# Performance work log

Hardware: AMD Instinct MI355X
Metric: run time of the kernel (lower is better)

## Reference

```python
import jax, jax.numpy as jnp
import numpy as np

B, DIM = 16384, 1024
H1, H2, H3 = 500, 200, 200


def setup_inputs() -> dict:
    key = jax.random.key(0)
    ks = jax.random.split(key, 16)
    s = 0.01
    return {
        "x": jax.random.normal(ks[0], (B, DIM), dtype=jnp.float32),
        "show_index": jax.random.randint(ks[1], (B,), 0, 100),
        "st": jax.random.normal(ks[2], (1000, 16), dtype=jnp.float32),
        # deep MLP params (shared across the two task heads, as in the source)
        "W1": jax.random.normal(ks[3], (DIM, H1), dtype=jnp.float32) * s,
        "b1": jnp.zeros((H1,), dtype=jnp.float32),
        "W2": jax.random.normal(ks[4], (H1, H2), dtype=jnp.float32) * s,
        "b2": jnp.zeros((H2,), dtype=jnp.float32),
        "W3": jax.random.normal(ks[5], (H2, H3), dtype=jnp.float32) * s,
        "b3": jnp.zeros((H3,), dtype=jnp.float32),
        # final sigmoid head on concat([emb(DIM), d3(H3)])
        "Wl": jax.random.normal(ks[6], (DIM + H3, 1), dtype=jnp.float32) * s,
        "bl": jnp.zeros((1,), dtype=jnp.float32),
        # per-(task, cross-layer) cross weights/biases: tf.random_normal stddev=0.01
        "cw": jax.random.normal(ks[7], (2, 3, DIM), dtype=jnp.float32) * s,
        "cb": jax.random.normal(ks[8], (2, 3, DIM), dtype=jnp.float32) * s,
    }


def reference(x, show_index, st, W1, b1, W2, b2, W3, b3, Wl, bl, cw, cb):
    # Deep part (same shared Dense layers each task -> compute once).
    d = jax.nn.relu(x @ W1 + b1)
    d = jax.nn.relu(d @ W2 + b2)
    d3 = jax.nn.relu(d @ W3 + b3)  # (B, H3)

    # cross_net: sum_i w[j] * x[b,i] * emb[b,j]  ==  x.sum(1) * emb[b,j] * w[j]
    # (collapsed form of the (B,dim,dim) outer product + axis-1 reduction)
    xsum = jnp.sum(x, axis=1, keepdims=True)  # (B, 1)
    preds = []
    for i in range(2):
        emb = x
        for j in range(3):
            emb = xsum * emb * cw[i, j] + cb[i, j] + x
        mid = jnp.concatenate([emb, d3], axis=-1)  # (B, DIM+H3)
        preds.append(jax.nn.sigmoid(mid @ Wl + bl))  # (B, 1)
    return tuple(preds)
```

## Files before the change

### kernel.cpp

```cpp
#include <hip/hip_runtime.h>
#include <hip/hip_bf16.h>
#include <math.h>

#define B_ROWS 16384
#define DIM 1024

typedef __attribute__((ext_vector_type(8))) short s16x8;
typedef __attribute__((ext_vector_type(4))) float f32x4;

static __device__ __forceinline__ unsigned short f2bf(float f) {
    union { float f; unsigned u; } v; v.f = f;
    unsigned r = v.u + 0x7FFF + ((v.u >> 16) & 1);
    return (unsigned short)(r >> 16);
}

static __device__ __forceinline__ unsigned cvt_pk_bf16(float lo, float hi) {
    unsigned r;
    asm volatile("v_cvt_pk_bf16_f32 %0, %1, %2" : "=v"(r) : "v"(lo), "v"(hi));
    return r;
}

static __device__ __forceinline__ void gload16(const unsigned short* g, unsigned short* l) {
    __builtin_amdgcn_global_load_lds(
        (const __attribute__((address_space(1))) unsigned int*)g,
        (__attribute__((address_space(3))) unsigned int*)l, 16, 0, 0);
}

__global__ __launch_bounds__(256) void prep(
    const float* __restrict__ W1, const float* __restrict__ W2,
    const float* __restrict__ W3,
    const float* __restrict__ cw, const float* __restrict__ cb,
    const float* __restrict__ Wl,
    unsigned short* __restrict__ W1b, unsigned short* __restrict__ W2b,
    unsigned short* __restrict__ W3b,
    float* __restrict__ czz) {
    __shared__ unsigned short tile[64][72];
    __shared__ float red[4][6];
    const int tid = threadIdx.x;
    const int blk = blockIdx.x;

    if (blk < 176) {
        const int w = blk;
        const float* src; unsigned short* dst;
        int kt, nt, Ksrc, Nsrc, ldDst;
        bool skipHi = false;
        if (w < 128)      { kt = w & 15;         nt = w >> 4;         src = W1; dst = W1b; Ksrc = 1024; Nsrc = 500; ldDst = 1024; skipHi = true; }
        else if (w < 160) { kt = (w - 128) & 7;  nt = (w - 128) >> 3; src = W2; dst = W2b; Ksrc = 500;  Nsrc = 200; ldDst = 512;  }
        else              { kt = (w - 160) & 3;  nt = (w - 160) >> 2; src = W3; dst = W3b; Ksrc = 200;  Nsrc = 200; ldDst = 256;  }
        const int k0 = kt << 6, n0 = nt << 6;
        {
            const int r = tid >> 2, c0 = (tid & 3) << 4;
            const int kk = k0 + r;
#pragma unroll
            for (int i = 0; i < 16; ++i) {
                const int nn = n0 + c0 + i;
                const float v = (kk < Ksrc && nn < Nsrc) ? src[(size_t)kk * Nsrc + nn] : 0.f;
                tile[r][c0 + i] = f2bf(v);
            }
        }
        __syncthreads();
        {
            const int n = tid >> 2, kc = (tid & 3) << 4;
            if (!(skipHi && (n0 + n) >= 500)) {
                unsigned short* o = dst + (size_t)(n0 + n) * ldDst + k0 + kc;
#pragma unroll
                for (int i = 0; i < 16; ++i) o[i] = tile[kc + i][n];
            }
        }
    } else if (blk == 176) {
#pragma unroll
        for (int q = 0; q < 4; ++q) {
            const int k = tid * 4 + q;
            const float wl = Wl[k];
            const float a1 = cw[k],         a2 = cw[1024 + k],  a3 = cw[2048 + k];
            const float d1_ = cw[3072 + k], d2_ = cw[4096 + k], d3_ = cw[5120 + k];
            W1b[(size_t)500 * 1024 + k] = f2bf(a1 * a2 * a3 * wl);
            W1b[(size_t)501 * 1024 + k] = f2bf(a2 * a3 * wl);
            W1b[(size_t)502 * 1024 + k] = f2bf(a3 * wl);
            W1b[(size_t)503 * 1024 + k] = f2bf(d1_ * d2_ * d3_ * wl);
            W1b[(size_t)504 * 1024 + k] = f2bf(d2_ * d3_ * wl);
            W1b[(size_t)505 * 1024 + k] = f2bf(d3_ * wl);
            W1b[(size_t)506 * 1024 + k] = f2bf(wl);
            W1b[(size_t)507 * 1024 + k] = 0x3F80;
            W1b[(size_t)508 * 1024 + k] = 0;
            W1b[(size_t)509 * 1024 + k] = 0;
            W1b[(size_t)510 * 1024 + k] = 0;
            W1b[(size_t)511 * 1024 + k] = 0;
        }
    } else {
        float c[6] = {0.f, 0.f, 0.f, 0.f, 0.f, 0.f};
#pragma unroll
        for (int q = 0; q < 4; ++q) {
            const int k = tid * 4 + q;
            const float wl = Wl[k];
            {
                const float w2 = cw[1024 + k], w3 = cw[2048 + k];
                const float b1 = cb[k], b2 = cb[1024 + k], b3 = cb[2048 + k];
                c[0] += w2 * w3 * b1 * wl;
                c[1] += w3 * b2 * wl;
                c[2] += b3 * wl;
            }
            {
                const float w2 = cw[4096 + k], w3 = cw[5120 + k];
                const float b1 = cb[3072 + k], b2 = cb[4096 + k], b3 = cb[5120 + k];
                c[3] += w2 * w3 * b1 * wl;
                c[4] += w3 * b2 * wl;
                c[5] += b3 * wl;
            }
        }
        const int lane = tid & 63, wv = tid >> 6;
#pragma unroll
        for (int j = 0; j < 6; ++j)
#pragma unroll
            for (int m = 1; m < 64; m <<= 1) c[j] += __shfl_xor(c[j], m, 64);
        if (lane == 0)
#pragma unroll
            for (int j = 0; j < 6; ++j) red[wv][j] = c[j];
        __syncthreads();
        if (tid < 6) czz[tid] = red[0][tid] + red[1][tid] + red[2][tid] + red[3][tid];
    }
}

template <int ROWS>
static __device__ __forceinline__ void stage_tile(
    const unsigned short* __restrict__ src, int K, int rowBase, int kt,
    unsigned short* lds, int w, int lane) {
    const int r8   = lane >> 3;
    const int slot = lane & 7;
#pragma unroll
    for (int q = 0; q < ROWS / 32; ++q) {
        const int blk   = q * 4 + w;
        const int row   = blk * 8 + r8;
        const int chunk = slot ^ (row & 7);
        const unsigned short* g = src + (size_t)(rowBase + row) * K + kt * 64 + chunk * 8;
        gload16(g, lds + blk * 512);
    }
}

template <int ROWS>
static __device__ __forceinline__ void stage8(
    const unsigned short* __restrict__ src, int K, int rowBase, int kt,
    unsigned short* lds, int w, int lane) {
    const int r8   = lane >> 3;
    const int slot = lane & 7;
#pragma unroll
    for (int q = 0; q < ROWS / 64; ++q) {
        const int blk   = q * 8 + w;
        const int row   = blk * 8 + r8;
        const int chunk = slot ^ (row & 7);
        const unsigned short* g = src + (size_t)(rowBase + row) * K + kt * 64 + chunk * 8;
        gload16(g, lds + blk * 512);
    }
}

__global__ __launch_bounds__(256) void gemm_xa(
    const float* __restrict__ X,
    const unsigned short* __restrict__ Bw,
    const float* __restrict__ bias,
    unsigned short* __restrict__ C,
    float* __restrict__ zparts) {
    constexpr int K = 1024, ldc = 512, BM = 128, nK = 16;
    __shared__ unsigned short As[2][BM * 64];
    __shared__ unsigned short Bs[2][128 * 64];

    const int tid  = threadIdx.x;
    const int lane = tid & 63;
    const int wid  = tid >> 6;
    const int wm   = wid >> 1;
    const int wn   = wid & 1;
    const int g    = lane >> 4;
    const int r16  = lane & 15;

    const int cpx = gridDim.x >> 3;
    const int swz = (blockIdx.x & 7) * cpx + (blockIdx.x >> 3);
    const int rowBase = (swz >> 2) * BM;
    const int colBase = (swz & 3) << 7;

    const int ar16 = tid >> 4;
    const int ak4  = tid & 15;
    const float* aSrc = X + (size_t)(rowBase + ar16) * K + ak4 * 4;

    float4 a_regs[8];

    f32x4 acc[4][4];
#pragma unroll
    for (int m = 0; m < 4; ++m)
#pragma unroll
        for (int n = 0; n < 4; ++n)
            acc[m][n] = (f32x4){0.f, 0.f, 0.f, 0.f};

    auto cvt_write_A = [&](unsigned short* dst) {
#pragma unroll
        for (int q = 0; q < 8; ++q) {
            const int row = q * 16 + ar16;
            const int ch  = (ak4 >> 1) ^ (row & 7);
            uint2 v;
            v.x = cvt_pk_bf16(a_regs[q].x, a_regs[q].y);
            v.y = cvt_pk_bf16(a_regs[q].z, a_regs[q].w);
            *(uint2*)((char*)dst + row * 128 + ch * 16 + (ak4 & 1) * 8) = v;
        }
    };
    auto issue_A = [&](int kt) {
#pragma unroll
        for (int q = 0; q < 8; ++q)
            a_regs[q] = *(const float4*)(aSrc + (size_t)q * 16 * K + kt * 64);
    };

    issue_A(0);
    asm volatile("" ::: "memory");
    stage_tile<128>(Bw, K, colBase, 0, Bs[0], wid, lane);
    asm volatile("" ::: "memory");
    cvt_write_A(As[0]);
    asm volatile("s_waitcnt vmcnt(0)" ::: "memory");
    asm volatile("s_waitcnt lgkmcnt(0)" ::: "memory");
    __builtin_amdgcn_s_barrier();
    asm volatile("" ::: "memory");

    for (int kt = 0; kt < nK; ++kt) {
        const int buf = kt & 1;
        if (kt + 1 < nK) {
            issue_A(kt + 1);
            asm volatile("" ::: "memory");
            stage_tile<128>(Bw, K, colBase, kt + 1, Bs[buf ^ 1], wid, lane);
            asm volatile("" ::: "memory");
        }

        const unsigned short* Ab = As[buf];
        const unsigned short* Bb = Bs[buf];
#pragma unroll
        for (int ks = 0; ks < 2; ++ks) {
            s16x8 af[4], bfr[4];
#pragma unroll
            for (int m = 0; m < 4; ++m) {
                const int row = wm * 64 + m * 16 + r16;
                const int off = ((ks * 4 + g) * 16) ^ ((row & 7) << 4);
                af[m] = *(const s16x8*)((const char*)Ab + row * 128 + off);
            }
#pragma unroll
            for (int n = 0; n < 4; ++n) {
                const int row = wn * 64 + n * 16 + r16;
                const int off = ((ks * 4 + g) * 16) ^ ((row & 7) << 4);
                bfr[n] = *(const s16x8*)((const char*)Bb + row * 128 + off);
            }
#pragma unroll
            for (int m = 0; m < 4; ++m)
#pragma unroll
                for (int n = 0; n < 4; ++n)
                    acc[m][n] = __builtin_amdgcn_mfma_f32_16x16x32_bf16(af[m], bfr[n], acc[m][n], 0, 0, 0);
        }

        if (kt + 1 < nK) {
            cvt_write_A(As[buf ^ 1]);
        }
        asm volatile("s_waitcnt vmcnt(0)" ::: "memory");
        asm volatile("s_waitcnt lgkmcnt(0)" ::: "memory");
        __builtin_amdgcn_s_barrier();
        asm volatile("" ::: "memory");
    }

#pragma unroll
    for (int n = 0; n < 4; ++n) {
        const int col = colBase + wn * 64 + n * 16 + r16;
        const float bv = (col < 500) ? bias[col] : 0.f;
        const unsigned pc = (unsigned)(col - 500);
#pragma unroll
        for (int m = 0; m < 4; ++m) {
            const int rowB = rowBase + wm * 64 + m * 16 + g * 4;
#pragma unroll
            for (int r = 0; r < 4; ++r) {
                const float raw = acc[m][n][r];
                float v = raw + bv;
                v = v > 0.f ? v : 0.f;
                C[(size_t)(rowB + r) * ldc + col] = f2bf(v);
                if (pc < 8u) zparts[(size_t)(rowB + r) * 8 + pc] = raw;
            }
        }
    }
}

__global__ __launch_bounds__(512) void tail_fused(
    const unsigned short* __restrict__ d1,
    const unsigned short* __restrict__ W2b,
    const float* __restrict__ b2,
    const unsigned short* __restrict__ W3b,
    const float* __restrict__ b3,
    const float* __restrict__ Wl,
    const float* __restrict__ bl,
    const float* __restrict__ zparts,
    const float* __restrict__ czz,
    float* __restrict__ out) {
    __shared__ unsigned short As[2][64 * 64];
    __shared__ unsigned short Bs[2][256 * 64];
    __shared__ unsigned short P[64 * 256];
    __shared__ float part[8][64];

    const int tid  = threadIdx.x;
    const int lane = tid & 63;
    const int wid  = tid >> 6;
    const int wm   = wid >> 2;
    const int wn   = wid & 3;
    const int g    = lane >> 4;
    const int r16  = lane & 15;
    const int rowBase = blockIdx.x << 6;

    f32x4 acc[2][4];
#pragma unroll
    for (int m = 0; m < 2; ++m)
#pragma unroll
        for (int n = 0; n < 4; ++n)
            acc[m][n] = (f32x4){0.f, 0.f, 0.f, 0.f};

    stage8<64>(d1, 512, rowBase, 0, As[0], wid, lane);
    stage8<256>(W2b, 512, 0, 0, Bs[0], wid, lane);

    for (int kt = 0; kt < 8; ++kt) {
        const int buf = kt & 1;
        if (kt + 1 < 8) {
            stage8<64>(d1, 512, rowBase, kt + 1, As[buf ^ 1], wid, lane);
            stage8<256>(W2b, 512, 0, kt + 1, Bs[buf ^ 1], wid, lane);
            asm volatile("s_waitcnt vmcnt(5)" ::: "memory");
        } else {
            asm volatile("s_waitcnt vmcnt(0)" ::: "memory");
        }
        __builtin_amdgcn_s_barrier();
        asm volatile("" ::: "memory");

        const unsigned short* Ab = As[buf];
        const unsigned short* Bb = Bs[buf];
#pragma unroll
        for (int ks = 0; ks < 2; ++ks) {
            s16x8 af[2], bfr[4];
#pragma unroll
            for (int m = 0; m < 2; ++m) {
                const int row = wm * 32 + m * 16 + r16;
                const int off = ((ks * 4 + g) * 16) ^ ((row & 7) << 4);
                af[m] = *(const s16x8*)((const char*)Ab + row * 128 + off);
            }
#pragma unroll
            for (int n = 0; n < 4; ++n) {
                const int row = wn * 64 + n * 16 + r16;
                const int off = ((ks * 4 + g) * 16) ^ ((row & 7) << 4);
                bfr[n] = *(const s16x8*)((const char*)Bb + row * 128 + off);
            }
#pragma unroll
            for (int m = 0; m < 2; ++m)
#pragma unroll
                for (int n = 0; n < 4; ++n)
                    acc[m][n] = __builtin_amdgcn_mfma_f32_16x16x32_bf16(af[m], bfr[n], acc[m][n], 0, 0, 0);
        }
        asm volatile("s_waitcnt lgkmcnt(0)" ::: "memory");
        __builtin_amdgcn_s_barrier();
        asm volatile("" ::: "memory");
    }

#pragma unroll
    for (int n = 0; n < 4; ++n) {
        const int col = wn * 64 + n * 16 + r16;
        const float bv = (col < 200) ? b2[col] : 0.f;
#pragma unroll
        for (int m = 0; m < 2; ++m) {
#pragma unroll
            for (int r = 0; r < 4; ++r) {
                const int row = wm * 32 + m * 16 + g * 4 + r;
                float v = acc[m][n][r] + bv;
                v = v > 0.f ? v : 0.f;
                const int byte = row * 512 + ((col * 2) ^ ((row & 7) << 4));
                *(unsigned short*)((char*)P + byte) = f2bf(v);
            }
        }
    }

    stage8<256>(W3b, 256, 0, 0, Bs[0], wid, lane);
    asm volatile("s_waitcnt lgkmcnt(0)" ::: "memory");
    __builtin_amdgcn_s_barrier();
    asm volatile("" ::: "memory");

    f32x4 acc2[2][4];
#pragma unroll
    for (int m = 0; m < 2; ++m)
#pragma unroll
        for (int n = 0; n < 4; ++n)
            acc2[m][n] = (f32x4){0.f, 0.f, 0.f, 0.f};

    for (int kt = 0; kt < 4; ++kt) {
        const int buf = kt & 1;
        if (kt + 1 < 4) {
            stage8<256>(W3b, 256, 0, kt + 1, Bs[buf ^ 1], wid, lane);
            asm volatile("s_waitcnt vmcnt(4)" ::: "memory");
        } else {
            asm volatile("s_waitcnt vmcnt(0)" ::: "memory");
        }
        __builtin_amdgcn_s_barrier();
        asm volatile("" ::: "memory");

        const unsigned short* Bb = Bs[buf];
#pragma unroll
        for (int ks = 0; ks < 2; ++ks) {
            s16x8 af[2], bfr[4];
#pragma unroll
            for (int m = 0; m < 2; ++m) {
                const int row = wm * 32 + m * 16 + r16;
                const int byte = row * 512 + ((kt * 128 + (ks * 4 + g) * 16) ^ ((row & 7) << 4));
                af[m] = *(const s16x8*)((const char*)P + byte);
            }
#pragma unroll
            for (int n = 0; n < 4; ++n) {
                const int row = wn * 64 + n * 16 + r16;
                const int off = ((ks * 4 + g) * 16) ^ ((row & 7) << 4);
                bfr[n] = *(const s16x8*)((const char*)Bb + row * 128 + off);
            }
#pragma unroll
            for (int m = 0; m < 2; ++m)
#pragma unroll
                for (int n = 0; n < 4; ++n)
                    acc2[m][n] = __builtin_amdgcn_mfma_f32_16x16x32_bf16(af[m], bfr[n], acc2[m][n], 0, 0, 0);
        }
        asm volatile("s_waitcnt lgkmcnt(0)" ::: "memory");
        __builtin_amdgcn_s_barrier();
        asm volatile("" ::: "memory");
    }

    float wlv[4], b3v[4];
#pragma unroll
    for (int n = 0; n < 4; ++n) {
        const int col = wn * 64 + n * 16 + r16;
        wlv[n] = (col < 200) ? Wl[1024 + col] : 0.f;
        b3v[n] = (col < 200) ? b3[col] : 0.f;
    }
#pragma unroll
    for (int m = 0; m < 2; ++m) {
#pragma unroll
        for (int r = 0; r < 4; ++r) {
            float s = 0.f;
#pragma unroll
            for (int n = 0; n < 4; ++n) {
                float v = acc2[m][n][r] + b3v[n];
                v = v > 0.f ? v : 0.f;
                s += v * wlv[n];
            }
            s += __shfl_xor(s, 1, 64);
            s += __shfl_xor(s, 2, 64);
            s += __shfl_xor(s, 4, 64);
            s += __shfl_xor(s, 8, 64);
            if (r16 == 0) part[wid][wm * 32 + m * 16 + g * 4 + r] = s;
        }
    }
    __syncthreads();

    if (tid < 64) {
        const int row = rowBase + tid;
        const int wmr = (tid >> 5) << 2;
        const float t = part[wmr][tid] + part[wmr + 1][tid] +
                        part[wmr + 2][tid] + part[wmr + 3][tid];
        const float blv = bl[0];
        const float* zp = zparts + (size_t)row * 8;
        float4 zpa = *(const float4*)(zp);
        float4 zpb = *(const float4*)(zp + 4);
        const float s = zpb.w;
        const float z0 = ((zpa.x * s + zpa.y + czz[0]) * s + zpa.z + czz[1]) * s
                         + zpb.z + czz[2] + t + blv;
        const float z1 = ((zpa.w * s + zpb.x + czz[3]) * s + zpb.y + czz[4]) * s
                         + zpb.z + czz[5] + t + blv;
        out[row]          = 1.f / (1.f + expf(-z0));
        out[B_ROWS + row] = 1.f / (1.f + expf(-z1));
    }
}

extern "C" void kernel_launch(void* const* d_in, const int* in_sizes, int n_in,
                              void* d_out, int out_size, void* d_ws, size_t ws_size,
                              hipStream_t stream) {
    const float* x  = (const float*)d_in[0];
    const float* W1 = (const float*)d_in[3];
    const float* b1 = (const float*)d_in[4];
    const float* W2 = (const float*)d_in[5];
    const float* b2 = (const float*)d_in[6];
    const float* W3 = (const float*)d_in[7];
    const float* b3 = (const float*)d_in[8];
    const float* Wl = (const float*)d_in[9];
    const float* bl = (const float*)d_in[10];
    const float* cw = (const float*)d_in[11];
    const float* cb = (const float*)d_in[12];
    float* out = (float*)d_out;

    unsigned short* d1  = (unsigned short*)d_ws;
    unsigned short* W1b = d1 + (size_t)16384 * 512;
    unsigned short* W2b = W1b + (size_t)512 * 1024;
    unsigned short* W3b = W2b + (size_t)256 * 512;
    float* zparts = (float*)(W3b + (size_t)256 * 256);
    float* czz = zparts + (size_t)16384 * 8;

    prep<<<178, 256, 0, stream>>>(W1, W2, W3, cw, cb, Wl, W1b, W2b, W3b, czz);

    gemm_xa<<<512, 256, 0, stream>>>(x, W1b, b1, d1, zparts);

    tail_fused<<<256, 512, 0, stream>>>(d1, W2b, b2, W3b, b3, Wl, bl,
                                        zparts, czz, out);
}
```

Baseline: 54.51 us.

## Prefetch A tiles two steps ahead with register double-banking in layer-1 GEMM

Restructures the first GEMM's main loop so fp32 A tiles are loaded into two alternating register banks two k-steps ahead. The bf16 conversion and LDS write of the next tile overlaps the MFMA work, and the loop is manually unrolled by two. The A load layout also changes from float4 per thread to 8 contiguous floats per thread, written to LDS as 16-byte stores. This aims to hide global-load latency of the fp32 activations, at the cost of doubling A staging registers, which may lower occupancy.

```diff
diff --git a/kernel.cpp b/kernel.cpp
--- a/kernel.cpp
+++ b/kernel.cpp
@@ -176,11 +176,11 @@
     const int rowBase = (swz >> 2) * BM;
     const int colBase = (swz & 3) << 7;
 
-    const int ar16 = tid >> 4;
-    const int ak4  = tid & 15;
-    const float* aSrc = X + (size_t)(rowBase + ar16) * K + ak4 * 4;
-
-    float4 a_regs[8];
+    const int arow = tid >> 3;
+    const int ak8  = tid & 7;
+    const float* aSrc = X + (size_t)(rowBase + arow) * K + ak8 * 8;
+
+    float4 bank0[8], bank1[8];
 
     f32x4 acc[4][4];
 #pragma unroll
@@ -189,74 +189,91 @@
         for (int n = 0; n < 4; ++n)
             acc[m][n] = (f32x4){0.f, 0.f, 0.f, 0.f};
 
-    auto cvt_write_A = [&](unsigned short* dst) {
-#pragma unroll
-        for (int q = 0; q < 8; ++q) {
-            const int row = q * 16 + ar16;
-            const int ch  = (ak4 >> 1) ^ (row & 7);
-            uint2 v;
-            v.x = cvt_pk_bf16(a_regs[q].x, a_regs[q].y);
-            v.y = cvt_pk_bf16(a_regs[q].z, a_regs[q].w);
-            *(uint2*)((char*)dst + row * 128 + ch * 16 + (ak4 & 1) * 8) = v;
-        }
-    };
-    auto issue_A = [&](int kt) {
-#pragma unroll
-        for (int q = 0; q < 8; ++q)
-            a_regs[q] = *(const float4*)(aSrc + (size_t)q * 16 * K + kt * 64);
-    };
-
-    issue_A(0);
+#define ISSUE_A(kt_, bank_)                                                   \
+    {                                                                         \
+        _Pragma("unroll")                                                     \
+        for (int q = 0; q < 4; ++q) {                                         \
+            const float* s_ = aSrc + (size_t)q * 32 * K + (kt_) * 64;         \
+            bank_[q * 2]     = *(const float4*)(s_);                          \
+            bank_[q * 2 + 1] = *(const float4*)(s_ + 4);                      \
+        }                                                                     \
+    }
+
+#define CVT_WRITE_A(bank_, dst_)                                              \
+    {                                                                         \
+        _Pragma("unroll")                                                     \
+        for (int q = 0; q < 4; ++q) {                                         \
+            const int row_ = q * 32 + arow;                                   \
+            const int ch_  = ak8 ^ (row_ & 7);                                \
+            uint4 v_;                                                         \
+            v_.x = cvt_pk_bf16(bank_[q * 2].x,     bank_[q * 2].y);           \
+            v_.y = cvt_pk_bf16(bank_[q * 2].z,     bank_[q * 2].w);           \
+            v_.z = cvt_pk_bf16(bank_[q * 2 + 1].x, bank_[q * 2 + 1].y);       \
+            v_.w = cvt_pk_bf16(bank_[q * 2 + 1].z, bank_[q * 2 + 1].w);       \
+            *(uint4*)((char*)(dst_) + row_ * 128 + ch_ * 16) = v_;            \
+        }                                                                     \
+    }
+
+#define COMPUTE(Ab_, Bb_)                                                     \
+    {                                                                         \
+        _Pragma("unroll")                                                     \
+        for (int ks = 0; ks < 2; ++ks) {                                      \
+            s16x8 af[4], bfr[4];                                              \
+            _Pragma("unroll")                                                 \
+            for (int m = 0; m < 4; ++m) {                                     \
+                const int row_ = wm * 64 + m * 16 + r16;                      \
+                const int off_ = ((ks * 4 + g) * 16) ^ ((row_ & 7) << 4);     \
+                af[m] = *(const s16x8*)((const char*)(Ab_) + row_ * 128 + off_); \
+            }                                                                 \
+            _Pragma("unroll")                                                 \
+            for (int n = 0; n < 4; ++n) {                                     \
+                const int row_ = wn * 64 + n * 16 + r16;                      \
+                const int off_ = ((ks * 4 + g) * 16) ^ ((row_ & 7) << 4);     \
+                bfr[n] = *(const s16x8*)((const char*)(Bb_) + row_ * 128 + off_); \
+            }                                                                 \
+            _Pragma("unroll")                                                 \
+            for (int m = 0; m < 4; ++m)                                       \
+                _Pragma("unroll")                                             \
+                for (int n = 0; n < 4; ++n)                                   \
+                    acc[m][n] = __builtin_amdgcn_mfma_f32_16x16x32_bf16(      \
+                        af[m], bfr[n], acc[m][n], 0, 0, 0);                   \
+        }                                                                     \
+    }
+
+    ISSUE_A(0, bank0);
+    asm volatile("" ::: "memory");
+    ISSUE_A(1, bank1);
     asm volatile("" ::: "memory");
     stage_tile<128>(Bw, K, colBase, 0, Bs[0], wid, lane);
+    asm volatile("s_waitcnt vmcnt(12)" ::: "memory");
+    CVT_WRITE_A(bank0, As[0]);
     asm volatile("" ::: "memory");
-    cvt_write_A(As[0]);
-    asm volatile("s_waitcnt vmcnt(0)" ::: "memory");
-    asm volatile("s_waitcnt lgkmcnt(0)" ::: "memory");
-    __builtin_amdgcn_s_barrier();
-    asm volatile("" ::: "memory");
-
-    for (int kt = 0; kt < nK; ++kt) {
-        const int buf = kt & 1;
-        if (kt + 1 < nK) {
-            issue_A(kt + 1);
-            asm volatile("" ::: "memory");
-            stage_tile<128>(Bw, K, colBase, kt + 1, Bs[buf ^ 1], wid, lane);
-            asm volatile("" ::: "memory");
-        }
-
-        const unsigned short* Ab = As[buf];
-        const unsigned short* Bb = Bs[buf];
-#pragma unroll
-        for (int ks = 0; ks < 2; ++ks) {
-            s16x8 af[4], bfr[4];
-#pragma unroll
-            for (int m = 0; m < 4; ++m) {
-                const int row = wm * 64 + m * 16 + r16;
-                const int off = ((ks * 4 + g) * 16) ^ ((row & 7) << 4);
-                af[m] = *(const s16x8*)((const char*)Ab + row * 128 + off);
-            }
-#pragma unroll
-            for (int n = 0; n < 4; ++n) {
-                const int row = wn * 64 + n * 16 + r16;
-                const int off = ((ks * 4 + g) * 16) ^ ((row & 7) << 4);
-                bfr[n] = *(const s16x8*)((const char*)Bb + row * 128 + off);
-            }
-#pragma unroll
-            for (int m = 0; m < 4; ++m)
-#pragma unroll
-                for (int n = 0; n < 4; ++n)
-                    acc[m][n] = __builtin_amdgcn_mfma_f32_16x16x32_bf16(af[m], bfr[n], acc[m][n], 0, 0, 0);
-        }
-
-        if (kt + 1 < nK) {
-            cvt_write_A(As[buf ^ 1]);
-        }
-        asm volatile("s_waitcnt vmcnt(0)" ::: "memory");
-        asm volatile("s_waitcnt lgkmcnt(0)" ::: "memory");
-        __builtin_amdgcn_s_barrier();
-        asm volatile("" ::: "memory");
-    }
+
+#define LOOP_ITER(kt_, bufA_, bufB_, oBufA_, oBufB_, ibank_, cbank_)          \
+    {                                                                         \
+        asm volatile("s_waitcnt vmcnt(0)" ::: "memory");                      \
+        __builtin_amdgcn_s_barrier();                                         \
+        asm volatile("" ::: "memory");                                        \
+        if ((kt_) + 2 < nK) { ISSUE_A((kt_) + 2, ibank_); }                   \
+        asm volatile("" ::: "memory");                                        \
+        if ((kt_) + 1 < nK)                                                   \
+            stage_tile<128>(Bw, K, colBase, (kt_) + 1, oBufB_, wid, lane);    \
+        asm volatile("" ::: "memory");                                        \
+        COMPUTE(bufA_, bufB_);                                                \
+        if ((kt_) + 1 < nK) { CVT_WRITE_A(cbank_, oBufA_); }                  \
+        asm volatile("s_waitcnt lgkmcnt(0)" ::: "memory");                    \
+        __builtin_amdgcn_s_barrier();                                         \
+        asm volatile("" ::: "memory");                                        \
+    }
+
+    for (int kt = 0; kt < nK; kt += 2) {
+        LOOP_ITER(kt,     As[0], Bs[0], As[1], Bs[1], bank0, bank1);
+        LOOP_ITER(kt + 1, As[1], Bs[1], As[0], Bs[0], bank1, bank0);
+    }
+#undef LOOP_ITER
+#undef COMPUTE
+#undef CVT_WRITE_A
+#undef ISSUE_A
 
 #pragma unroll
     for (int n = 0; n < 4; ++n) {
```

Result: faster. 52.02 us (-4.6%).

## Pre-convert x to bf16 in prep and stage both GEMM operands via direct LDS loads

Applied to the files above, without the earlier changes.

Adds a pass in the prep kernel that converts the fp32 input x to a bf16 copy in workspace. The first-layer GEMM then loads both A and B tiles with global_load_lds instead of fp32 register loads followed by in-register conversion and LDS writes. The epilogue also stages the output tile in LDS so global stores are coalesced 16-byte writes. This removes register pressure and conversion work from the GEMM main loop, but it adds an extra full read of x and a 32 MB bf16 write and re-read through memory.

```diff
diff --git a/kernel.cpp b/kernel.cpp
--- a/kernel.cpp
+++ b/kernel.cpp
@@ -14,12 +14,6 @@
     return (unsigned short)(r >> 16);
 }
 
-static __device__ __forceinline__ unsigned cvt_pk_bf16(float lo, float hi) {
-    unsigned r;
-    asm volatile("v_cvt_pk_bf16_f32 %0, %1, %2" : "=v"(r) : "v"(lo), "v"(hi));
-    return r;
-}
-
 static __device__ __forceinline__ void gload16(const unsigned short* g, unsigned short* l) {
     __builtin_amdgcn_global_load_lds(
         (const __attribute__((address_space(1))) unsigned int*)g,
@@ -27,6 +21,7 @@
 }
 
 __global__ __launch_bounds__(256) void prep(
+    const float* __restrict__ x, unsigned short* __restrict__ xb,
     const float* __restrict__ W1, const float* __restrict__ W2,
     const float* __restrict__ W3,
     const float* __restrict__ cw, const float* __restrict__ cb,
@@ -39,8 +34,19 @@
     const int tid = threadIdx.x;
     const int blk = blockIdx.x;
 
-    if (blk < 176) {
-        const int w = blk;
+    if (blk < 4096) {
+        const float* src = x + (size_t)blk * 4096;
+        unsigned short* dst = xb + (size_t)blk * 4096;
+#pragma unroll
+        for (int r = 0; r < 4; ++r) {
+            float4 f = *(const float4*)(src + r * 1024 + tid * 4);
+            short4 h;
+            h.x = (short)f2bf(f.x); h.y = (short)f2bf(f.y);
+            h.z = (short)f2bf(f.z); h.w = (short)f2bf(f.w);
+            *(short4*)(dst + r * 1024 + tid * 4) = h;
+        }
+    } else if (blk < 4272) {
+        const int w = blk - 4096;
         const float* src; unsigned short* dst;
         int kt, nt, Ksrc, Nsrc, ldDst;
         bool skipHi = false;
@@ -67,7 +73,7 @@
                 for (int i = 0; i < 16; ++i) o[i] = tile[kc + i][n];
             }
         }
-    } else if (blk == 176) {
+    } else if (blk == 4272) {
 #pragma unroll
         for (int q = 0; q < 4; ++q) {
             const int k = tid * 4 + q;
@@ -153,8 +159,8 @@
     }
 }
 
-__global__ __launch_bounds__(256) void gemm_xa(
-    const float* __restrict__ X,
+__global__ __launch_bounds__(256) void gemm_bf16(
+    const unsigned short* __restrict__ A,
     const unsigned short* __restrict__ Bw,
     const float* __restrict__ bias,
     unsigned short* __restrict__ C,
@@ -176,12 +182,6 @@
     const int rowBase = (swz >> 2) * BM;
     const int colBase = (swz & 3) << 7;
 
-    const int ar16 = tid >> 4;
-    const int ak4  = tid & 15;
-    const float* aSrc = X + (size_t)(rowBase + ar16) * K + ak4 * 4;
-
-    float4 a_regs[8];
-
     f32x4 acc[4][4];
 #pragma unroll
     for (int m = 0; m < 4; ++m)
@@ -189,41 +189,19 @@
         for (int n = 0; n < 4; ++n)
             acc[m][n] = (f32x4){0.f, 0.f, 0.f, 0.f};
 
-    auto cvt_write_A = [&](unsigned short* dst) {
-#pragma unroll
-        for (int q = 0; q < 8; ++q) {
-            const int row = q * 16 + ar16;
-            const int ch  = (ak4 >> 1) ^ (row & 7);
-            uint2 v;
-            v.x = cvt_pk_bf16(a_regs[q].x, a_regs[q].y);
-            v.y = cvt_pk_bf16(a_regs[q].z, a_regs[q].w);
-            *(uint2*)((char*)dst + row * 128 + ch * 16 + (ak4 & 1) * 8) = v;
-        }
-    };
-    auto issue_A = [&](int kt) {
-#pragma unroll
-        for (int q = 0; q < 8; ++q)
-            a_regs[q] = *(const float4*)(aSrc + (size_t)q * 16 * K + kt * 64);
-    };
-
-    issue_A(0);
-    asm volatile("" ::: "memory");
+    stage_tile<BM>(A, K, rowBase, 0, As[0], wid, lane);
     stage_tile<128>(Bw, K, colBase, 0, Bs[0], wid, lane);
-    asm volatile("" ::: "memory");
-    cvt_write_A(As[0]);
     asm volatile("s_waitcnt vmcnt(0)" ::: "memory");
-    asm volatile("s_waitcnt lgkmcnt(0)" ::: "memory");
     __builtin_amdgcn_s_barrier();
     asm volatile("" ::: "memory");
 
     for (int kt = 0; kt < nK; ++kt) {
         const int buf = kt & 1;
         if (kt + 1 < nK) {
-            issue_A(kt + 1);
-            asm volatile("" ::: "memory");
+            stage_tile<BM>(A, K, rowBase, kt + 1, As[buf ^ 1], wid, lane);
             stage_tile<128>(Bw, K, colBase, kt + 1, Bs[buf ^ 1], wid, lane);
-            asm volatile("" ::: "memory");
-        }
+        }
+        asm volatile("" ::: "memory");
 
         const unsigned short* Ab = As[buf];
         const unsigned short* Bb = Bs[buf];
@@ -249,32 +227,43 @@
                     acc[m][n] = __builtin_amdgcn_mfma_f32_16x16x32_bf16(af[m], bfr[n], acc[m][n], 0, 0, 0);
         }
 
-        if (kt + 1 < nK) {
-            cvt_write_A(As[buf ^ 1]);
-        }
-        asm volatile("s_waitcnt vmcnt(0)" ::: "memory");
-        asm volatile("s_waitcnt lgkmcnt(0)" ::: "memory");
+        if (kt + 1 < nK)
+            asm volatile("s_waitcnt vmcnt(0)" ::: "memory");
         __builtin_amdgcn_s_barrier();
         asm volatile("" ::: "memory");
     }
 
+    unsigned short* Cb = As[0];
 #pragma unroll
     for (int n = 0; n < 4; ++n) {
         const int col = colBase + wn * 64 + n * 16 + r16;
+        const int lcol = wn * 64 + n * 16 + r16;
         const float bv = (col < 500) ? bias[col] : 0.f;
         const unsigned pc = (unsigned)(col - 500);
 #pragma unroll
         for (int m = 0; m < 4; ++m) {
-            const int rowB = rowBase + wm * 64 + m * 16 + g * 4;
+            const int lrow = wm * 64 + m * 16 + g * 4;
 #pragma unroll
             for (int r = 0; r < 4; ++r) {
                 const float raw = acc[m][n][r];
+                if (pc < 8u) zparts[(size_t)(rowBase + lrow + r) * 8 + pc] = raw;
                 float v = raw + bv;
                 v = v > 0.f ? v : 0.f;
-                C[(size_t)(rowB + r) * ldc + col] = f2bf(v);
-                if (pc < 8u) zparts[(size_t)(rowB + r) * 8 + pc] = raw;
-            }
-        }
+                Cb[(lrow + r) * 128 + lcol] = f2bf(v);
+            }
+        }
+    }
+    __syncthreads();
+
+    {
+        const int row  = tid >> 1;
+        const int half = tid & 1;
+        const uint4* s = (const uint4*)(Cb + row * 128 + half * 64);
+        uint4* d = (uint4*)(C + (size_t)(rowBase + row) * ldc + colBase + half * 64);
+        d[0] = s[0];
+        d[1] = s[1];
+        d[2] = s[2];
+        d[3] = s[3];
     }
 }
 
@@ -482,16 +471,18 @@
     const float* cb = (const float*)d_in[12];
     float* out = (float*)d_out;
 
-    unsigned short* d1  = (unsigned short*)d_ws;
+    unsigned short* xb  = (unsigned short*)d_ws;
+    unsigned short* d1  = xb + (size_t)16384 * 1024;
     unsigned short* W1b = d1 + (size_t)16384 * 512;
     unsigned short* W2b = W1b + (size_t)512 * 1024;
     unsigned short* W3b = W2b + (size_t)256 * 512;
     float* zparts = (float*)(W3b + (size_t)256 * 256);
     float* czz = zparts + (size_t)16384 * 8;
 
-    prep<<<178, 256, 0, stream>>>(W1, W2, W3, cw, cb, Wl, W1b, W2b, W3b, czz);
-
-    gemm_xa<<<512, 256, 0, stream>>>(x, W1b, b1, d1, zparts);
+    prep<<<4274, 256, 0, stream>>>(x, xb, W1, W2, W3, cw, cb, Wl,
+                                   W1b, W2b, W3b, czz);
+
+    gemm_bf16<<<512, 256, 0, stream>>>(xb, W1b, b1, d1, zparts);
 
     tail_fused<<<256, 512, 0, stream>>>(d1, W2b, b2, W3b, b3, Wl, bl,
                                         zparts, czz, out);
```

Result: slower. 61.46 us (+12.7%).

## Use 512-thread blocks in first GEMM and stage output through LDS

Applied to the files above, without the earlier changes.

The first GEMM goes from 4 to 8 waves per block. Each wave now owns a 64x32 output sub-tile instead of 64x64, and the B tile is staged with stage8. Each thread loads one row segment of fp32 X as four float4 loads and writes two 16-byte bf16 chunks into LDS. The epilogue writes the bf16 results into LDS first, then copies them to global memory with coalesced 16-byte stores. This is meant to raise latency hiding and improve store coalescing, at the cost of an extra barrier and fewer MFMAs per wave.

```diff
diff --git a/kernel.cpp b/kernel.cpp
--- a/kernel.cpp
+++ b/kernel.cpp
@@ -122,22 +122,6 @@
 }
 
 template <int ROWS>
-static __device__ __forceinline__ void stage_tile(
-    const unsigned short* __restrict__ src, int K, int rowBase, int kt,
-    unsigned short* lds, int w, int lane) {
-    const int r8   = lane >> 3;
-    const int slot = lane & 7;
-#pragma unroll
-    for (int q = 0; q < ROWS / 32; ++q) {
-        const int blk   = q * 4 + w;
-        const int row   = blk * 8 + r8;
-        const int chunk = slot ^ (row & 7);
-        const unsigned short* g = src + (size_t)(rowBase + row) * K + kt * 64 + chunk * 8;
-        gload16(g, lds + blk * 512);
-    }
-}
-
-template <int ROWS>
 static __device__ __forceinline__ void stage8(
     const unsigned short* __restrict__ src, int K, int rowBase, int kt,
     unsigned short* lds, int w, int lane) {
@@ -153,62 +137,67 @@
     }
 }
 
-__global__ __launch_bounds__(256) void gemm_xa(
+__global__ __launch_bounds__(512, 4) void gemm_xa(
     const float* __restrict__ X,
     const unsigned short* __restrict__ Bw,
     const float* __restrict__ bias,
     unsigned short* __restrict__ C,
     float* __restrict__ zparts) {
-    constexpr int K = 1024, ldc = 512, BM = 128, nK = 16;
-    __shared__ unsigned short As[2][BM * 64];
+    constexpr int K = 1024, ldc = 512, nK = 16;
+    __shared__ unsigned short As[2][128 * 64];
     __shared__ unsigned short Bs[2][128 * 64];
 
     const int tid  = threadIdx.x;
     const int lane = tid & 63;
     const int wid  = tid >> 6;
-    const int wm   = wid >> 1;
-    const int wn   = wid & 1;
+    const int wm   = wid >> 2;
+    const int wn   = wid & 3;
     const int g    = lane >> 4;
     const int r16  = lane & 15;
 
     const int cpx = gridDim.x >> 3;
     const int swz = (blockIdx.x & 7) * cpx + (blockIdx.x >> 3);
-    const int rowBase = (swz >> 2) * BM;
+    const int rowBase = (swz >> 2) << 7;
     const int colBase = (swz & 3) << 7;
 
-    const int ar16 = tid >> 4;
-    const int ak4  = tid & 15;
-    const float* aSrc = X + (size_t)(rowBase + ar16) * K + ak4 * 4;
-
-    float4 a_regs[8];
-
-    f32x4 acc[4][4];
+    const int arow = tid >> 2;
+    const int ak   = (tid & 3) << 4;
+    const float* aSrc = X + (size_t)(rowBase + arow) * K + ak;
+
+    float4 a_regs[4];
+
+    f32x4 acc[4][2];
 #pragma unroll
     for (int m = 0; m < 4; ++m)
 #pragma unroll
-        for (int n = 0; n < 4; ++n)
+        for (int n = 0; n < 2; ++n)
             acc[m][n] = (f32x4){0.f, 0.f, 0.f, 0.f};
 
+    auto issue_A = [&](int kt) {
+#pragma unroll
+        for (int q = 0; q < 4; ++q)
+            a_regs[q] = *(const float4*)(aSrc + kt * 64 + q * 4);
+    };
     auto cvt_write_A = [&](unsigned short* dst) {
-#pragma unroll
-        for (int q = 0; q < 8; ++q) {
-            const int row = q * 16 + ar16;
-            const int ch  = (ak4 >> 1) ^ (row & 7);
-            uint2 v;
-            v.x = cvt_pk_bf16(a_regs[q].x, a_regs[q].y);
-            v.y = cvt_pk_bf16(a_regs[q].z, a_regs[q].w);
-            *(uint2*)((char*)dst + row * 128 + ch * 16 + (ak4 & 1) * 8) = v;
-        }
-    };
-    auto issue_A = [&](int kt) {
-#pragma unroll
-        for (int q = 0; q < 8; ++q)
-            a_regs[q] = *(const float4*)(aSrc + (size_t)q * 16 * K + kt * 64);
+        const int cb = (tid & 3) << 1;
+        uint4 v0, v1;
+        v0.x = cvt_pk_bf16(a_regs[0].x, a_regs[0].y);
+        v0.y = cvt_pk_bf16(a_regs[0].z, a_regs[0].w);
+        v0.z = cvt_pk_bf16(a_regs[1].x, a_regs[1].y);
+        v0.w = cvt_pk_bf16(a_regs[1].z, a_regs[1].w);
+        v1.x = cvt_pk_bf16(a_regs[2].x, a_regs[2].y);
+        v1.y = cvt_pk_bf16(a_regs[2].z, a_regs[2].w);
+        v1.z = cvt_pk_bf16(a_regs[3].x, a_regs[3].y);
+        v1.w = cvt_pk_bf16(a_regs[3].z, a_regs[3].w);
+        const int ch0 = (cb + 0) ^ (arow & 7);
+        const int ch1 = (cb + 1) ^ (arow & 7);
+        *(uint4*)((char*)dst + arow * 128 + ch0 * 16) = v0;
+        *(uint4*)((char*)dst + arow * 128 + ch1 * 16) = v1;
     };
 
     issue_A(0);
     asm volatile("" ::: "memory");
-    stage_tile<128>(Bw, K, colBase, 0, Bs[0], wid, lane);
+    stage8<128>(Bw, K, colBase, 0, Bs[0], wid, lane);
     asm volatile("" ::: "memory");
     cvt_write_A(As[0]);
     asm volatile("s_waitcnt vmcnt(0)" ::: "memory");
@@ -221,7 +210,7 @@
         if (kt + 1 < nK) {
             issue_A(kt + 1);
             asm volatile("" ::: "memory");
-            stage_tile<128>(Bw, K, colBase, kt + 1, Bs[buf ^ 1], wid, lane);
+            stage8<128>(Bw, K, colBase, kt + 1, Bs[buf ^ 1], wid, lane);
             asm volatile("" ::: "memory");
         }
 
@@ -229,7 +218,7 @@
         const unsigned short* Bb = Bs[buf];
 #pragma unroll
         for (int ks = 0; ks < 2; ++ks) {
-            s16x8 af[4], bfr[4];
+            s16x8 af[4], bfr[2];
 #pragma unroll
             for (int m = 0; m < 4; ++m) {
                 const int row = wm * 64 + m * 16 + r16;
@@ -237,15 +226,15 @@
                 af[m] = *(const s16x8*)((const char*)Ab + row * 128 + off);
             }
 #pragma unroll
-            for (int n = 0; n < 4; ++n) {
-                const int row = wn * 64 + n * 16 + r16;
+            for (int n = 0; n < 2; ++n) {
+                const int row = wn * 32 + n * 16 + r16;
                 const int off = ((ks * 4 + g) * 16) ^ ((row & 7) << 4);
                 bfr[n] = *(const s16x8*)((const char*)Bb + row * 128 + off);
             }
 #pragma unroll
             for (int m = 0; m < 4; ++m)
 #pragma unroll
-                for (int n = 0; n < 4; ++n)
+                for (int n = 0; n < 2; ++n)
                     acc[m][n] = __builtin_amdgcn_mfma_f32_16x16x32_bf16(af[m], bfr[n], acc[m][n], 0, 0, 0);
         }
 
@@ -258,23 +247,35 @@
         asm volatile("" ::: "memory");
     }
 
-#pragma unroll
-    for (int n = 0; n < 4; ++n) {
-        const int col = colBase + wn * 64 + n * 16 + r16;
+    unsigned short* Cb = As[0];
+#pragma unroll
+    for (int n = 0; n < 2; ++n) {
+        const int lcol = wn * 32 + n * 16 + r16;
+        const int col = colBase + lcol;
         const float bv = (col < 500) ? bias[col] : 0.f;
         const unsigned pc = (unsigned)(col - 500);
 #pragma unroll
         for (int m = 0; m < 4; ++m) {
-            const int rowB = rowBase + wm * 64 + m * 16 + g * 4;
+            const int lrow = wm * 64 + m * 16 + g * 4;
 #pragma unroll
             for (int r = 0; r < 4; ++r) {
                 const float raw = acc[m][n][r];
+                if (pc < 8u) zparts[(size_t)(rowBase + lrow + r) * 8 + pc] = raw;
                 float v = raw + bv;
                 v = v > 0.f ? v : 0.f;
-                C[(size_t)(rowB + r) * ldc + col] = f2bf(v);
-                if (pc < 8u) zparts[(size_t)(rowB + r) * 8 + pc] = raw;
-            }
-        }
+                Cb[(lrow + r) * 128 + lcol] = f2bf(v);
+            }
+        }
+    }
+    __syncthreads();
+
+    {
+        const int row = tid >> 2;
+        const int q   = tid & 3;
+        const uint4* s = (const uint4*)(Cb + row * 128 + q * 32);
+        uint4* d = (uint4*)(C + (size_t)(rowBase + row) * ldc + colBase + q * 32);
+        d[0] = s[0];
+        d[1] = s[1];
     }
 }
 
@@ -491,7 +492,7 @@
 
     prep<<<178, 256, 0, stream>>>(W1, W2, W3, cw, cb, Wl, W1b, W2b, W3b, czz);
 
-    gemm_xa<<<512, 256, 0, stream>>>(x, W1b, b1, d1, zparts);
+    gemm_xa<<<512, 512, 0, stream>>>(x, W1b, b1, d1, zparts);
 
     tail_fused<<<256, 512, 0, stream>>>(d1, W2b, b2, W3b, b3, Wl, bl,
                                         zparts, czz, out);
```

New measurement: 55.31 us. About the same (+1.5%).
